# Kernel optimization log

Measured on AMD Instinct MI355X. Metric: run time of the kernel, lower is better.

The kernel has to match this reference:

```python
import jax, jax.numpy as jnp
import numpy as np

E = 8      # num routed experts
H = 1024   # hidden_size
I = 1408   # moe_intermediate_size
T = 2048   # tokens (batch*seq flattened)
K = 2      # top_k experts per token


def setup_inputs() -> dict:
    key = jax.random.key(0)
    k1, k2, k3, k4, k5 = jax.random.split(key, 5)
    x = jax.random.normal(k1, (T, H), dtype=jnp.float32)
    expert_ids = jax.random.randint(k2, (T, K), 0, E, dtype=jnp.int64)
    routing_weights = jax.random.uniform(k3, (T, K), dtype=jnp.float32)
    # kaiming_uniform_(a=sqrt(5)) on 2D tensor -> bound = 1/sqrt(fan_in), fan_in = dim1
    b1 = 1.0 / np.sqrt(2 * I)
    w1 = jax.random.uniform(k4, (E * H, 2 * I), dtype=jnp.float32, minval=-b1, maxval=b1)
    b2 = 1.0 / np.sqrt(H)
    w2 = jax.random.uniform(k5, (E * I, H), dtype=jnp.float32, minval=-b2, maxval=b2)
    return {"x": x, "expert_ids": expert_ids, "routing_weights": routing_weights,
            "w1": w1, "w2": w2}


def reference(x, expert_ids, routing_weights, w1, w2):
    # Fused routed MLP: per token, for each of its top-k experts e with gate p:
    #   out += p * (silu(x @ W1_gate[e]) * (x @ W1_up[e])) @ W2[e]
    w1r = w1.reshape(E, H, 2 * I)   # fused gate+up per expert
    w2r = w2.reshape(E, I, H)       # down proj per expert

    h = jnp.einsum('th,ehi->eti', x, w1r)           # [E, T, 2I]
    gate, up = h[..., :I], h[..., I:]
    act = jax.nn.silu(gate) * up                    # [E, T, I]
    y = jnp.einsum('eti,eih->eth', act, w2r)        # [E, T, H]

    # combine weights: [T, E] = sum over the k slots of onehot(expert)*routing_weight
    disp = jnp.sum(jax.nn.one_hot(expert_ids, E, dtype=x.dtype)
                   * routing_weights[..., None], axis=1)  # [T, E]
    out = jnp.einsum('eth,te->th', y, disp)         # [T, H]
    return out
```

## Files before the change

### kernel.cpp

```cpp
#include <hip/hip_runtime.h>
#include <hip/hip_bf16.h>
#include <math.h>

#define E    8
#define H    1024
#define I2   2816
#define II   1408
#define T    2048
#define KTOP 2
#define NP   (T * KTOP)

#define BM   128
#define BK   32
#define BNA  64
#define BN2  128
#define GX   40

typedef __attribute__((ext_vector_type(8))) short  short8v;
typedef __attribute__((ext_vector_type(4))) float  f32x4;
typedef __attribute__((ext_vector_type(8))) unsigned short ushort8;

__device__ __forceinline__ void gload16(void* lds, const void* g) {
    __builtin_amdgcn_global_load_lds((const __attribute__((address_space(1))) unsigned int*)g,
                                     (__attribute__((address_space(3))) unsigned int*)lds,
                                     16, 0, 0);
}

__global__ void route_kernel(const int* __restrict__ ids, const float* __restrict__ rw,
                             int* __restrict__ tok, float* __restrict__ wt,
                             int* __restrict__ seg_off, int* __restrict__ tile_off)
{
    __shared__ int cnt[E];
    __shared__ int base[E + 1];
    __shared__ int pos[E];
    int tid = threadIdx.x;
    if (tid < E) { cnt[tid] = 0; pos[tid] = 0; }
    __syncthreads();
    for (int p = tid; p < NP; p += blockDim.x) atomicAdd(&cnt[ids[p]], 1);
    __syncthreads();
    if (tid == 0) {
        int s = 0;
        for (int e = 0; e < E; ++e) { base[e] = s; s += cnt[e]; }
        base[E] = s;
    }
    __syncthreads();
    for (int p = tid; p < NP; p += blockDim.x) {
        int e = ids[p];
        int q = base[e] + atomicAdd(&pos[e], 1);
        tok[q] = p >> 1;
        wt[q]  = rw[p];
    }
    if (tid == 0) {
        int s = 0;
        for (int e = 0; e < E; ++e) {
            seg_off[e]  = base[e];
            tile_off[e] = s;
            s += (cnt[e] + BM - 1) / BM;
        }
        seg_off[E]  = base[E];
        tile_off[E] = s;
    }
}

__global__ void cvt_x(const float* __restrict__ src, __hip_bfloat16* __restrict__ dst, int n)
{
    int i = (blockIdx.x * blockDim.x + threadIdx.x) * 8;
    if (i >= n) return;
    float4 a = *(const float4*)(src + i);
    float4 b = *(const float4*)(src + i + 4);
    alignas(16) __hip_bfloat16 t[8];
    t[0] = __float2bfloat16(a.x); t[1] = __float2bfloat16(a.y);
    t[2] = __float2bfloat16(a.z); t[3] = __float2bfloat16(a.w);
    t[4] = __float2bfloat16(b.x); t[5] = __float2bfloat16(b.y);
    t[6] = __float2bfloat16(b.z); t[7] = __float2bfloat16(b.w);
    *(ushort8*)(dst + i) = *(ushort8*)t;
}

__launch_bounds__(256)
__global__ void transpose_cvt(const float* __restrict__ src, __hip_bfloat16* __restrict__ dst,
                              int K, int N)
{
    __shared__ float tile[64][65];
    int e  = blockIdx.z;
    int n0 = blockIdx.x * 64;
    int k0 = blockIdx.y * 64;
    int tid = threadIdx.x;

    const float* s = src + (size_t)e * K * N + (size_t)k0 * N + n0;
    int kr = tid >> 2;
    int nc = (tid & 3) * 16;
    const float* srow = s + (size_t)kr * N + nc;
#pragma unroll
    for (int i = 0; i < 4; ++i) {
        float4 v = *(const float4*)(srow + i * 4);
        tile[kr][nc + i * 4 + 0] = v.x;
        tile[kr][nc + i * 4 + 1] = v.y;
        tile[kr][nc + i * 4 + 2] = v.z;
        tile[kr][nc + i * 4 + 3] = v.w;
    }
    __syncthreads();
    int nr = tid >> 2;
    int kc = (tid & 3) * 16;
    alignas(16) __hip_bfloat16 tmp[16];
#pragma unroll
    for (int i = 0; i < 16; ++i) tmp[i] = __float2bfloat16(tile[kc + i][nr]);
    __hip_bfloat16* drow = dst + (size_t)e * K * N + (size_t)(n0 + nr) * K + k0 + kc;
    *(ushort8*)(drow)     = *(ushort8*)tmp;
    *(ushort8*)(drow + 8) = *(ushort8*)(tmp + 8);
}

__launch_bounds__(256, 2)
__global__ void gemm1_silu(const __hip_bfloat16* __restrict__ xb,
                           const __hip_bfloat16* __restrict__ w1t,
                           const int* __restrict__ tok,
                           const int* __restrict__ seg_off,
                           const int* __restrict__ tile_off,
                           __hip_bfloat16* __restrict__ act)
{
    __shared__ __align__(16) __hip_bfloat16 As[BM * BK];
    __shared__ __align__(16) __hip_bfloat16 Bg[BNA * BK];
    __shared__ __align__(16) __hip_bfloat16 Bu[BNA * BK];
    __shared__ int tokS[BM];

    int bx = blockIdx.x;
    if (bx >= tile_off[E]) return;
    int e = 0;
#pragma unroll
    for (int i = 1; i < E; ++i) if (bx >= tile_off[i]) e = i;
    int row0 = seg_off[e] + (bx - tile_off[e]) * BM;
    int rend = seg_off[e + 1];
    int jb   = blockIdx.y * BNA;

    int tid = threadIdx.x;
    if (tid < BM) {
        int gr = row0 + tid;
        tokS[tid] = tok[gr < NP ? gr : NP - 1];
    }
    __syncthreads();

    int arow = tid >> 2;
    int aoff = (tid & 3) * 16;
    const char* xB  = (const char*)xb;
    const char* w1B = (const char*)(w1t + (size_t)e * I2 * H);
    const char* srcA0 = xB + (size_t)tokS[arow]      * 2048 + aoff;
    const char* srcA1 = xB + (size_t)tokS[arow + 64] * 2048 + aoff;
    const char* srcG  = w1B + (size_t)(jb + arow)      * 2048 + aoff;
    const char* srcU  = w1B + (size_t)(II + jb + arow) * 2048 + aoff;
    __hip_bfloat16* dA0 = &As[tid * 8];
    __hip_bfloat16* dA1 = &As[2048 + tid * 8];
    __hip_bfloat16* dG  = &Bg[tid * 8];
    __hip_bfloat16* dU  = &Bu[tid * 8];

    int lane = tid & 63;
    int w  = tid >> 6;
    int wm = w >> 1, wn = w & 1;
    int fr = lane & 15;
    int kc = lane >> 4;

    f32x4 accg[4][2] = {};
    f32x4 accu[4][2] = {};
    const short8v* Asv = (const short8v*)As;
    const short8v* Bgv = (const short8v*)Bg;
    const short8v* Buv = (const short8v*)Bu;

    for (int k0 = 0; k0 < H; k0 += BK) {
        gload16(dA0, srcA0);
        gload16(dA1, srcA1);
        gload16(dG, srcG);
        gload16(dU, srcU);
        srcA0 += 64; srcA1 += 64; srcG += 64; srcU += 64;
        __syncthreads();

        short8v a[4], g[2], u[2];
#pragma unroll
        for (int m = 0; m < 4; ++m)
            a[m] = Asv[(wm * 64 + m * 16 + fr) * 4 + kc];
#pragma unroll
        for (int n = 0; n < 2; ++n) {
            g[n] = Bgv[(wn * 32 + n * 16 + fr) * 4 + kc];
            u[n] = Buv[(wn * 32 + n * 16 + fr) * 4 + kc];
        }
#pragma unroll
        for (int m = 0; m < 4; ++m)
#pragma unroll
            for (int n = 0; n < 2; ++n) {
                accg[m][n] = __builtin_amdgcn_mfma_f32_16x16x32_bf16(a[m], g[n], accg[m][n], 0, 0, 0);
                accu[m][n] = __builtin_amdgcn_mfma_f32_16x16x32_bf16(a[m], u[n], accu[m][n], 0, 0, 0);
            }
        __syncthreads();
    }

#pragma unroll
    for (int m = 0; m < 4; ++m)
#pragma unroll
        for (int n = 0; n < 2; ++n) {
            int col = jb + wn * 32 + n * 16 + fr;
#pragma unroll
            for (int j = 0; j < 4; ++j) {
                int gr = row0 + wm * 64 + m * 16 + kc * 4 + j;
                if (gr < rend) {
                    float gg = accg[m][n][j];
                    float s  = gg / (1.0f + __expf(-gg));
                    act[(size_t)gr * II + col] = __float2bfloat16(s * accu[m][n][j]);
                }
            }
        }
}

__launch_bounds__(256, 2)
__global__ void gemm2_scatter(const __hip_bfloat16* __restrict__ act,
                              const __hip_bfloat16* __restrict__ w2t,
                              const int* __restrict__ tok,
                              const float* __restrict__ wt,
                              const int* __restrict__ seg_off,
                              const int* __restrict__ tile_off,
                              float* __restrict__ out)
{
    __shared__ __align__(16) __hip_bfloat16 As[BM * BK];
    __shared__ __align__(16) __hip_bfloat16 Bs[BN2 * BK];
    __shared__ int   tokS[BM];
    __shared__ float wtS[BM];

    int bx = blockIdx.x;
    if (bx >= tile_off[E]) return;
    int e = 0;
#pragma unroll
    for (int i = 1; i < E; ++i) if (bx >= tile_off[i]) e = i;
    int row0 = seg_off[e] + (bx - tile_off[e]) * BM;
    int rend = seg_off[e + 1];
    int nb   = blockIdx.y * BN2;

    int tid = threadIdx.x;
    if (tid < BM) {
        int gr = row0 + tid; gr = gr < NP ? gr : NP - 1;
        tokS[tid] = tok[gr];
        wtS[tid]  = wt[gr];
    }
    __syncthreads();

    int arow = tid >> 2;
    int aoff = (tid & 3) * 16;
    const char* actB = (const char*)act;
    const char* w2B  = (const char*)(w2t + (size_t)e * H * II);
    int r0c = row0 + arow;       r0c = r0c < NP ? r0c : NP - 1;
    int r1c = row0 + arow + 64;  r1c = r1c < NP ? r1c : NP - 1;
    const char* srcA0 = actB + (size_t)r0c * 2816 + aoff;
    const char* srcA1 = actB + (size_t)r1c * 2816 + aoff;
    const char* srcB0 = w2B + (size_t)(nb + arow)      * 2816 + aoff;
    const char* srcB1 = w2B + (size_t)(nb + arow + 64) * 2816 + aoff;
    __hip_bfloat16* dA0 = &As[tid * 8];
    __hip_bfloat16* dA1 = &As[2048 + tid * 8];
    __hip_bfloat16* dB0 = &Bs[tid * 8];
    __hip_bfloat16* dB1 = &Bs[2048 + tid * 8];

    int lane = tid & 63;
    int w  = tid >> 6;
    int wm = w >> 1, wn = w & 1;
    int fr = lane & 15;
    int kc = lane >> 4;

    f32x4 acc[4][4] = {};
    const short8v* Asv = (const short8v*)As;
    const short8v* Bsv = (const short8v*)Bs;

    for (int k0 = 0; k0 < II; k0 += BK) {
        gload16(dA0, srcA0);
        gload16(dA1, srcA1);
        gload16(dB0, srcB0);
        gload16(dB1, srcB1);
        srcA0 += 64; srcA1 += 64; srcB0 += 64; srcB1 += 64;
        __syncthreads();

        short8v a[4], b[4];
#pragma unroll
        for (int m = 0; m < 4; ++m)
            a[m] = Asv[(wm * 64 + m * 16 + fr) * 4 + kc];
#pragma unroll
        for (int n = 0; n < 4; ++n)
            b[n] = Bsv[(wn * 64 + n * 16 + fr) * 4 + kc];
#pragma unroll
        for (int m = 0; m < 4; ++m)
#pragma unroll
            for (int n = 0; n < 4; ++n)
                acc[m][n] = __builtin_amdgcn_mfma_f32_16x16x32_bf16(a[m], b[n], acc[m][n], 0, 0, 0);
        __syncthreads();
    }

#pragma unroll
    for (int m = 0; m < 4; ++m)
#pragma unroll
        for (int n = 0; n < 4; ++n) {
            int col = nb + wn * 64 + n * 16 + fr;
#pragma unroll
            for (int j = 0; j < 4; ++j) {
                int lr = wm * 64 + m * 16 + kc * 4 + j;
                int gr = row0 + lr;
                if (gr < rend)
                    atomicAdd(&out[(size_t)tokS[lr] * H + col], wtS[lr] * acc[m][n][j]);
            }
        }
}

extern "C" void kernel_launch(void* const* d_in, const int* in_sizes, int n_in,
                              void* d_out, int out_size, void* d_ws, size_t ws_size,
                              hipStream_t stream)
{
    const float* x   = (const float*)d_in[0];
    const int*   ids = (const int*)d_in[1];
    const float* rw  = (const float*)d_in[2];
    const float* w1  = (const float*)d_in[3];
    const float* w2  = (const float*)d_in[4];
    float*       out = (float*)d_out;

    char* ws = (char*)d_ws;
    int*   tok  = (int*)ws;
    float* wt   = (float*)(ws + 16384);
    int*   seg  = (int*)(ws + 32768);
    int*   tile = (int*)(ws + 32768 + 64);
    __hip_bfloat16* xb  = (__hip_bfloat16*)(ws + 65536);
    __hip_bfloat16* w1t = (__hip_bfloat16*)(ws + 65536 + 4194304);
    __hip_bfloat16* w2t = (__hip_bfloat16*)(ws + 65536 + 4194304 + 46137344);
    __hip_bfloat16* act = (__hip_bfloat16*)(ws + 65536 + 4194304 + 46137344 + 23068672);

    hipMemsetAsync(d_out, 0, (size_t)out_size * sizeof(float), stream);

    cvt_x<<<(T * H) / (256 * 8), 256, 0, stream>>>(x, xb, T * H);
    transpose_cvt<<<dim3(I2 / 64, H / 64, E), 256, 0, stream>>>(w1, w1t, H, I2);
    transpose_cvt<<<dim3(H / 64, II / 64, E), 256, 0, stream>>>(w2, w2t, II, H);
    route_kernel<<<1, 256, 0, stream>>>(ids, rw, tok, wt, seg, tile);

    gemm1_silu<<<dim3(GX, II / BNA), 256, 0, stream>>>(xb, w1t, tok, seg, tile, act);
    gemm2_scatter<<<dim3(GX, H / BN2), 256, 0, stream>>>(act, w2t, tok, wt, seg, tile, out);
}
```

Measured before the change: 303.4 us.

## Fuse prep kernels into one launch and replace atomic scatter with gather combine

Merges the x conversion, both weight transpose-converts and the routing step into a single prep kernel, and drops the output memset. The second GEMM now writes unweighted per-slot rows to a float buffer, and a new gather kernel combines each token's two expert rows with their routing weights. This removes launch overhead and the float atomics on the output. In exchange it adds an extra 16 MB write and read of the intermediate y buffer.

```diff
diff --git a/kernel.cpp b/kernel.cpp
--- a/kernel.cpp
+++ b/kernel.cpp
@@ -16,6 +16,13 @@
 #define BN2  128
 #define GX   40
 
+#define CVT_BLKS   1024
+#define TW1_PER_E  (44 * 16)
+#define TW1_BLKS   (TW1_PER_E * E)
+#define TW2_PER_E  (16 * 22)
+#define TW2_BLKS   (TW2_PER_E * E)
+#define PREP_BLKS  (CVT_BLKS + TW1_BLKS + TW2_BLKS + 1)
+
 typedef __attribute__((ext_vector_type(8))) short  short8v;
 typedef __attribute__((ext_vector_type(4))) float  f32x4;
 typedef __attribute__((ext_vector_type(8))) unsigned short ushort8;
@@ -26,66 +33,16 @@
                                      16, 0, 0);
 }
 
-__global__ void route_kernel(const int* __restrict__ ids, const float* __restrict__ rw,
-                             int* __restrict__ tok, float* __restrict__ wt,
-                             int* __restrict__ seg_off, int* __restrict__ tile_off)
-{
-    __shared__ int cnt[E];
-    __shared__ int base[E + 1];
-    __shared__ int pos[E];
-    int tid = threadIdx.x;
-    if (tid < E) { cnt[tid] = 0; pos[tid] = 0; }
-    __syncthreads();
-    for (int p = tid; p < NP; p += blockDim.x) atomicAdd(&cnt[ids[p]], 1);
-    __syncthreads();
-    if (tid == 0) {
-        int s = 0;
-        for (int e = 0; e < E; ++e) { base[e] = s; s += cnt[e]; }
-        base[E] = s;
-    }
-    __syncthreads();
-    for (int p = tid; p < NP; p += blockDim.x) {
-        int e = ids[p];
-        int q = base[e] + atomicAdd(&pos[e], 1);
-        tok[q] = p >> 1;
-        wt[q]  = rw[p];
-    }
-    if (tid == 0) {
-        int s = 0;
-        for (int e = 0; e < E; ++e) {
-            seg_off[e]  = base[e];
-            tile_off[e] = s;
-            s += (cnt[e] + BM - 1) / BM;
-        }
-        seg_off[E]  = base[E];
-        tile_off[E] = s;
-    }
-}
-
-__global__ void cvt_x(const float* __restrict__ src, __hip_bfloat16* __restrict__ dst, int n)
-{
-    int i = (blockIdx.x * blockDim.x + threadIdx.x) * 8;
-    if (i >= n) return;
-    float4 a = *(const float4*)(src + i);
-    float4 b = *(const float4*)(src + i + 4);
-    alignas(16) __hip_bfloat16 t[8];
-    t[0] = __float2bfloat16(a.x); t[1] = __float2bfloat16(a.y);
-    t[2] = __float2bfloat16(a.z); t[3] = __float2bfloat16(a.w);
-    t[4] = __float2bfloat16(b.x); t[5] = __float2bfloat16(b.y);
-    t[6] = __float2bfloat16(b.z); t[7] = __float2bfloat16(b.w);
-    *(ushort8*)(dst + i) = *(ushort8*)t;
-}
-
-__launch_bounds__(256)
-__global__ void transpose_cvt(const float* __restrict__ src, __hip_bfloat16* __restrict__ dst,
-                              int K, int N)
-{
-    __shared__ float tile[64][65];
-    int e  = blockIdx.z;
-    int n0 = blockIdx.x * 64;
-    int k0 = blockIdx.y * 64;
-    int tid = threadIdx.x;
-
+union PrepShared {
+    float tile[64][65];
+    struct { int cnt[E]; int base[E + 1]; int pos[E]; } rt;
+};
+
+__device__ __forceinline__ void transpose_tile(const float* __restrict__ src,
+                                               __hip_bfloat16* __restrict__ dst,
+                                               int e, int n0, int k0, int K, int N,
+                                               PrepShared& sh, int tid)
+{
     const float* s = src + (size_t)e * K * N + (size_t)k0 * N + n0;
     int kr = tid >> 2;
     int nc = (tid & 3) * 16;
@@ -93,20 +50,86 @@
 #pragma unroll
     for (int i = 0; i < 4; ++i) {
         float4 v = *(const float4*)(srow + i * 4);
-        tile[kr][nc + i * 4 + 0] = v.x;
-        tile[kr][nc + i * 4 + 1] = v.y;
-        tile[kr][nc + i * 4 + 2] = v.z;
-        tile[kr][nc + i * 4 + 3] = v.w;
+        sh.tile[kr][nc + i * 4 + 0] = v.x;
+        sh.tile[kr][nc + i * 4 + 1] = v.y;
+        sh.tile[kr][nc + i * 4 + 2] = v.z;
+        sh.tile[kr][nc + i * 4 + 3] = v.w;
     }
     __syncthreads();
     int nr = tid >> 2;
     int kc = (tid & 3) * 16;
     alignas(16) __hip_bfloat16 tmp[16];
 #pragma unroll
-    for (int i = 0; i < 16; ++i) tmp[i] = __float2bfloat16(tile[kc + i][nr]);
+    for (int i = 0; i < 16; ++i) tmp[i] = __float2bfloat16(sh.tile[kc + i][nr]);
     __hip_bfloat16* drow = dst + (size_t)e * K * N + (size_t)(n0 + nr) * K + k0 + kc;
     *(ushort8*)(drow)     = *(ushort8*)tmp;
     *(ushort8*)(drow + 8) = *(ushort8*)(tmp + 8);
+}
+
+__launch_bounds__(256)
+__global__ void prep_kernel(const float* __restrict__ x, const float* __restrict__ w1,
+                            const float* __restrict__ w2, const int* __restrict__ ids,
+                            __hip_bfloat16* __restrict__ xb,
+                            __hip_bfloat16* __restrict__ w1t,
+                            __hip_bfloat16* __restrict__ w2t,
+                            int* __restrict__ tok, int* __restrict__ inv,
+                            int* __restrict__ seg_off, int* __restrict__ tile_off)
+{
+    __shared__ PrepShared sh;
+    int tid = threadIdx.x;
+    int b = blockIdx.x;
+
+    if (b < CVT_BLKS) {
+        int i = (b * 256 + tid) * 8;
+        float4 a = *(const float4*)(x + i);
+        float4 c = *(const float4*)(x + i + 4);
+        alignas(16) __hip_bfloat16 t[8];
+        t[0] = __float2bfloat16(a.x); t[1] = __float2bfloat16(a.y);
+        t[2] = __float2bfloat16(a.z); t[3] = __float2bfloat16(a.w);
+        t[4] = __float2bfloat16(c.x); t[5] = __float2bfloat16(c.y);
+        t[6] = __float2bfloat16(c.z); t[7] = __float2bfloat16(c.w);
+        *(ushort8*)(xb + i) = *(ushort8*)t;
+        return;
+    }
+    b -= CVT_BLKS;
+    if (b < TW1_BLKS) {
+        int e = b / TW1_PER_E, r = b % TW1_PER_E;
+        transpose_tile(w1, w1t, e, (r % 44) * 64, (r / 44) * 64, H, I2, sh, tid);
+        return;
+    }
+    b -= TW1_BLKS;
+    if (b < TW2_BLKS) {
+        int e = b / TW2_PER_E, r = b % TW2_PER_E;
+        transpose_tile(w2, w2t, e, (r % 16) * 64, (r / 16) * 64, II, H, sh, tid);
+        return;
+    }
+
+    if (tid < E) { sh.rt.cnt[tid] = 0; sh.rt.pos[tid] = 0; }
+    __syncthreads();
+    for (int p = tid; p < NP; p += 256) atomicAdd(&sh.rt.cnt[ids[p]], 1);
+    __syncthreads();
+    if (tid == 0) {
+        int s = 0;
+        for (int e = 0; e < E; ++e) { sh.rt.base[e] = s; s += sh.rt.cnt[e]; }
+        sh.rt.base[E] = s;
+    }
+    __syncthreads();
+    for (int p = tid; p < NP; p += 256) {
+        int e = ids[p];
+        int q = sh.rt.base[e] + atomicAdd(&sh.rt.pos[e], 1);
+        tok[q] = p >> 1;
+        inv[p] = q;
+    }
+    if (tid == 0) {
+        int s = 0;
+        for (int e = 0; e < E; ++e) {
+            seg_off[e]  = sh.rt.base[e];
+            tile_off[e] = s;
+            s += (sh.rt.cnt[e] + BM - 1) / BM;
+        }
+        seg_off[E]  = sh.rt.base[E];
+        tile_off[E] = s;
+    }
 }
 
 __launch_bounds__(256, 2)
@@ -208,18 +231,14 @@
 }
 
 __launch_bounds__(256, 2)
-__global__ void gemm2_scatter(const __hip_bfloat16* __restrict__ act,
-                              const __hip_bfloat16* __restrict__ w2t,
-                              const int* __restrict__ tok,
-                              const float* __restrict__ wt,
-                              const int* __restrict__ seg_off,
-                              const int* __restrict__ tile_off,
-                              float* __restrict__ out)
+__global__ void gemm2(const __hip_bfloat16* __restrict__ act,
+                      const __hip_bfloat16* __restrict__ w2t,
+                      const int* __restrict__ seg_off,
+                      const int* __restrict__ tile_off,
+                      float* __restrict__ y)
 {
     __shared__ __align__(16) __hip_bfloat16 As[BM * BK];
     __shared__ __align__(16) __hip_bfloat16 Bs[BN2 * BK];
-    __shared__ int   tokS[BM];
-    __shared__ float wtS[BM];
 
     int bx = blockIdx.x;
     if (bx >= tile_off[E]) return;
@@ -231,13 +250,6 @@
     int nb   = blockIdx.y * BN2;
 
     int tid = threadIdx.x;
-    if (tid < BM) {
-        int gr = row0 + tid; gr = gr < NP ? gr : NP - 1;
-        tokS[tid] = tok[gr];
-        wtS[tid]  = wt[gr];
-    }
-    __syncthreads();
-
     int arow = tid >> 2;
     int aoff = (tid & 3) * 16;
     const char* actB = (const char*)act;
@@ -296,9 +308,27 @@
                 int lr = wm * 64 + m * 16 + kc * 4 + j;
                 int gr = row0 + lr;
                 if (gr < rend)
-                    atomicAdd(&out[(size_t)tokS[lr] * H + col], wtS[lr] * acc[m][n][j]);
+                    y[(size_t)gr * H + col] = acc[m][n][j];
             }
         }
+}
+
+__global__ void gather_out(const float* __restrict__ y, const int* __restrict__ inv,
+                           const float* __restrict__ rw, float* __restrict__ out)
+{
+    int gid = blockIdx.x * 256 + threadIdx.x;
+    int t = gid >> 8;
+    int c = (gid & 255) * 4;
+    int q0 = inv[2 * t], q1 = inv[2 * t + 1];
+    float w0 = rw[2 * t], w1 = rw[2 * t + 1];
+    float4 a = *(const float4*)(y + (size_t)q0 * H + c);
+    float4 b = *(const float4*)(y + (size_t)q1 * H + c);
+    float4 o;
+    o.x = w0 * a.x + w1 * b.x;
+    o.y = w0 * a.y + w1 * b.y;
+    o.z = w0 * a.z + w1 * b.z;
+    o.w = w0 * a.w + w1 * b.w;
+    *(float4*)(out + (size_t)t * H + c) = o;
 }
 
 extern "C" void kernel_launch(void* const* d_in, const int* in_sizes, int n_in,
@@ -314,21 +344,19 @@
 
     char* ws = (char*)d_ws;
     int*   tok  = (int*)ws;
-    float* wt   = (float*)(ws + 16384);
+    int*   inv  = (int*)(ws + 16384);
     int*   seg  = (int*)(ws + 32768);
     int*   tile = (int*)(ws + 32768 + 64);
     __hip_bfloat16* xb  = (__hip_bfloat16*)(ws + 65536);
-    __hip_bfloat16* w1t = (__hip_bfloat16*)(ws + 65536 + 4194304);
-    __hip_bfloat16* w2t = (__hip_bfloat16*)(ws + 65536 + 4194304 + 46137344);
-    __hip_bfloat16* act = (__hip_bfloat16*)(ws + 65536 + 4194304 + 46137344 + 23068672);
-
-    hipMemsetAsync(d_out, 0, (size_t)out_size * sizeof(float), stream);
-
-    cvt_x<<<(T * H) / (256 * 8), 256, 0, stream>>>(x, xb, T * H);
-    transpose_cvt<<<dim3(I2 / 64, H / 64, E), 256, 0, stream>>>(w1, w1t, H, I2);
-    transpose_cvt<<<dim3(H / 64, II / 64, E), 256, 0, stream>>>(w2, w2t, II, H);
-    route_kernel<<<1, 256, 0, stream>>>(ids, rw, tok, wt, seg, tile);
+    __hip_bfloat16* w1t = (__hip_bfloat16*)(ws + 4259840);
+    __hip_bfloat16* w2t = (__hip_bfloat16*)(ws + 50397184);
+    __hip_bfloat16* act = (__hip_bfloat16*)(ws + 73465856);
+    float*          y   = (float*)(ws + 85000192);
+
+    prep_kernel<<<PREP_BLKS, 256, 0, stream>>>(x, w1, w2, ids, xb, w1t, w2t,
+                                               tok, inv, seg, tile);
 
     gemm1_silu<<<dim3(GX, II / BNA), 256, 0, stream>>>(xb, w1t, tok, seg, tile, act);
-    gemm2_scatter<<<dim3(GX, H / BN2), 256, 0, stream>>>(act, w2t, tok, wt, seg, tile, out);
-}
+    gemm2<<<dim3(GX, H / BN2), 256, 0, stream>>>(act, w2t, seg, tile, y);
+    gather_out<<<(T * H) / (256 * 4), 256, 0, stream>>>(y, inv, rw, out);
+}
```

New measurement: 278.0 us. 8.4% less time.
